# Optimization experiments

Hardware: AMD Instinct MI355X
Metric: run time of the kernel (lower is better)

The kernel has to match this reference:

```python
import jax, jax.numpy as jnp
import numpy as np

BN_EPS = 1e-5
LEAKY_SLOPE = 0.01

def setup_inputs() -> dict:
    key = jax.random.key(0)
    ks = jax.random.split(key, 8)
    B, N, C, D = 8, 2048, 128, 32  # batch, points, inchannels, outchannels
    s = 0.05
    return {
        "x": jax.random.normal(ks[0], (B, N, C), dtype=jnp.float32),
        "Wq": jax.random.normal(ks[1], (D, C), dtype=jnp.float32) * s,
        "Wk": jax.random.normal(ks[2], (D, C), dtype=jnp.float32) * s,
        "Wv": jax.random.normal(ks[3], (C, C), dtype=jnp.float32) * s,
        "Wp": jax.random.normal(ks[4], (C, C), dtype=jnp.float32) * s,
        "bn_gamma": jnp.ones((C,), dtype=jnp.float32),
        "bn_beta": jnp.zeros((C,), dtype=jnp.float32),
        "bn_mean": jax.random.normal(ks[5], (C,), dtype=jnp.float32) * 0.01,
        "bn_var": jnp.abs(jax.random.normal(ks[6], (C,), dtype=jnp.float32)) * 0.1 + 0.9,
    }

def reference(x, Wq, Wk, Wv, Wp, bn_gamma, bn_beta, bn_mean, bn_var):
    # x: [B, N, C]; 1x1 Conv1d == per-point linear map
    q = jnp.einsum('bnc,dc->bnd', x, Wq)          # [B, N, D]
    k = jnp.einsum('bnc,dc->bnd', x, Wk)          # [B, N, D]
    v = jnp.einsum('bnc,oc->bno', x, Wv)          # [B, N, C]
    energy = jnp.einsum('bnd,bmd->bnm', q, k)     # [B, Nq, Nk]
    # offset-attention: softmax over the QUERY axis (dim=1), then L1-renorm over keys
    attn = jax.nn.softmax(energy, axis=1)
    attn = attn / (1e-9 + attn.sum(axis=-1, keepdims=True))
    x_r = jnp.einsum('bnm,bmc->bnc', attn, v)     # [B, N, C]
    # project(x - x_r): 1x1 conv + BatchNorm (eval, running stats) + LeakyReLU; dropout p=0
    d = x - x_r
    y = jnp.einsum('bnc,oc->bno', d, Wp)
    y = (y - bn_mean) * (bn_gamma / jnp.sqrt(bn_var + BN_EPS)) + bn_beta
    y = jnp.where(y >= 0, y, LEAKY_SLOPE * y)
    return y + x
```

## Files before the change

kernel.cpp:

```cpp
#include <hip/hip_runtime.h>
#include <stdint.h>

#define BB 8
#define NN 2048
#define CC 128
#define DD 32
#define LOG2E 1.44269504088896340736f

typedef __attribute__((ext_vector_type(8))) short short8;
typedef __attribute__((ext_vector_type(4))) short short4v;
typedef __attribute__((ext_vector_type(4))) float f32x4;

#define MFMA(a,b,c) __builtin_amdgcn_mfma_f32_16x16x32_bf16(a,b,c,0,0,0)

__device__ __forceinline__ short f2b(float f){
  uint32_t u = __float_as_uint(f);
  uint32_t r = (u + 0x7fffu + ((u >> 16) & 1u)) >> 16;
  return (short)r;
}

__global__ void k_pack(const float* __restrict__ Wq, const float* __restrict__ Wk,
                       const float* __restrict__ Wv, const float* __restrict__ Wp,
                       const float* __restrict__ g, const float* __restrict__ bt,
                       const float* __restrict__ mu, const float* __restrict__ vr,
                       short* __restrict__ wqkv, short* __restrict__ wp,
                       float* __restrict__ scale, float* __restrict__ shift){
  int i = blockIdx.x*256 + threadIdx.x;
  if (i < 192*128){
    int r = i >> 7, c = i & 127;
    float w = (r < 32) ? Wq[r*128+c] : (r < 64) ? Wk[(r-32)*128+c] : Wv[(r-64)*128+c];
    wqkv[i] = f2b(w);
  }
  if (i < 128*128) wp[i] = f2b(Wp[i]);
  if (i < 128){
    float s = g[i] * rsqrtf(vr[i] + 1e-5f);
    scale[i] = s;
    shift[i] = bt[i] - mu[i]*s;
  }
}

__global__ __launch_bounds__(256,4) void k_qkv(const float* __restrict__ x, const short* __restrict__ wqkv,
    short* __restrict__ qb, short* __restrict__ kb, short* __restrict__ vt){
  const int tid = threadIdx.x;
  const int wv = tid >> 6, l = tid & 63, lrow = l & 15, lg = l >> 4;
  const int r0 = blockIdx.x*32 + (wv & 1)*16;
  const int base = (wv >> 1)*6;
  const float* xr = x + (long)(r0 + lrow)*CC;
  short8 a[4];
  #pragma unroll
  for (int ks=0; ks<4; ks++){
    f32x4 u0 = *(const f32x4*)(xr + ks*32 + lg*8);
    f32x4 u1 = *(const f32x4*)(xr + ks*32 + lg*8 + 4);
    short8 t;
    #pragma unroll
    for (int j=0;j<4;j++){ t[j] = f2b(u0[j]); t[4+j] = f2b(u1[j]); }
    a[ks] = t;
  }
  f32x4 acc[6];
  #pragma unroll
  for (int i=0;i<6;i++) acc[i] = f32x4{0.f,0.f,0.f,0.f};
  #pragma unroll
  for (int of=0; of<6; of++){
    #pragma unroll
    for (int ks=0; ks<4; ks++){
      short8 bfr = *(const short8*)(wqkv + ((base+of)*16 + lrow)*CC + ks*32 + lg*8);
      acc[of] = MFMA(a[ks], bfr, acc[of]);
    }
  }
  const int b = r0 / NN, nin = r0 % NN;
  #pragma unroll
  for (int of=0; of<6; of++){
    const int oo = base + of;
    const int o = oo*16 + lrow;
    if (oo < 2){
      #pragma unroll
      for (int rr=0; rr<4; rr++) qb[(long)(r0 + lg*4 + rr)*DD + o] = f2b(acc[of][rr]*LOG2E);
    } else if (oo < 4){
      #pragma unroll
      for (int rr=0; rr<4; rr++) kb[(long)(r0 + lg*4 + rr)*DD + (o-32)] = f2b(acc[of][rr]);
    } else {
      short4v s;
      #pragma unroll
      for (int rr=0; rr<4; rr++) s[rr] = f2b(acc[of][rr]);
      *(short4v*)(vt + (long)(b*CC + (o-64))*NN + nin + lg*4) = s;
    }
  }
}

__global__ __launch_bounds__(256,4) void k_colsum(const short* __restrict__ qb, const short* __restrict__ kb,
                                                  float* __restrict__ csum){
  const int tid = threadIdx.x;
  const int wv = tid >> 6, l = tid & 63, lrow = l & 15, lg = l >> 4;
  const int b = blockIdx.x >> 7;
  const int q = (blockIdx.x >> 5) & 3;
  const int m0 = (blockIdx.x & 31)*64 + wv*16;
  short8 afr = *(const short8*)(kb + (long)(b*NN + m0 + lrow)*DD + lg*8);
  const short* qbase = qb + (long)b*NN*DD;
  float sum[4] = {0.f,0.f,0.f,0.f};
  f32x4 z = {0.f,0.f,0.f,0.f};
  const int nbeg = q*512, nend = nbeg + 512;
  #pragma unroll 4
  for (int n0=nbeg; n0<nend; n0+=16){
    short8 bfr = *(const short8*)(qbase + (long)(n0 + lrow)*DD + lg*8);
    f32x4 e = MFMA(afr, bfr, z);
    #pragma unroll
    for (int r=0;r<4;r++) sum[r] += exp2f(e[r]);
  }
  #pragma unroll
  for (int mask=1; mask<16; mask<<=1){
    #pragma unroll
    for (int r=0;r<4;r++) sum[r] += __shfl_xor(sum[r], mask);
  }
  if (lrow == 0){
    #pragma unroll
    for (int r=0;r<4;r++) csum[q*(BB*NN) + b*NN + m0 + lg*4 + r] = sum[r];
  }
}

__global__ __launch_bounds__(256,4) void k_attn(const short* __restrict__ qb,
    const short* __restrict__ kb, const short* __restrict__ vt, const float* __restrict__ csum,
    float* __restrict__ accP, float* __restrict__ Lp){
  __shared__ __align__(16) short lds[17408];
  const int tid = threadIdx.x;
  const int wv = tid >> 6, l = tid & 63, lrow = l & 15, lg = l >> 4;
  const int b = blockIdx.x >> 7;
  const int quarter = (blockIdx.x >> 5) & 3;
  const int rt = blockIdx.x & 31;
  const int n0 = rt*64 + wv*16;
  short8 qfr = *(const short8*)(qb + (long)(b*NN + n0 + lrow)*DD + lg*8);
  const short* kbb = kb + (long)b*NN*DD;
  const short* vtb = vt + (long)b*CC*NN;
  float* sinvl = (float*)(lds + 16384);

  const int mbase = quarter*512;
  {
    const float* c0 = csum + b*NN + mbase;
    #pragma unroll
    for (int i=tid; i<512; i+=256){
      float s = c0[i] + c0[i + BB*NN] + c0[i + 2*BB*NN] + c0[i + 3*BB*NN];
      sinvl[i] = __builtin_amdgcn_rcpf(s);
    }
  }

  f32x4 acc[8];
  #pragma unroll
  for (int i=0;i<8;i++) acc[i] = f32x4{0.f,0.f,0.f,0.f};
  float L[4] = {0.f,0.f,0.f,0.f};

  short8 sv[4]; short8 sk[2];
  const int cr = tid >> 1, hf = tid & 1;

  auto loadT = [&](int m0){
    const short* s = vtb + (long)cr*NN + m0 + hf*32;
    sv[0] = *(const short8*)(s);
    sv[1] = *(const short8*)(s+8);
    sv[2] = *(const short8*)(s+16);
    sv[3] = *(const short8*)(s+24);
    if (tid < 128){
      const short* s2 = kbb + (long)(m0 + cr)*DD + hf*16;
      sk[0] = *(const short8*)(s2);
      sk[1] = *(const short8*)(s2+8);
    }
  };
  auto storeT = [&](){
    short* vt_t = lds;
    *(short8*)(vt_t + cr*72 + hf*32 + 0)  = sv[0];
    *(short8*)(vt_t + cr*72 + hf*32 + 8)  = sv[1];
    *(short8*)(vt_t + cr*72 + hf*32 + 16) = sv[2];
    *(short8*)(vt_t + cr*72 + hf*32 + 24) = sv[3];
    if (tid < 128){
      short* kb_t = vt_t + 9216;
      *(short8*)(kb_t + cr*40 + hf*16 + 0) = sk[0];
      *(short8*)(kb_t + cr*40 + hf*16 + 8) = sk[1];
    }
  };

  loadT(mbase);
  storeT();
  __syncthreads();

  short* pl = lds + 11776 + wv*1152;
  f32x4 z = {0.f,0.f,0.f,0.f};
  for (int it=0; it<8; it++){
    const int m0 = mbase + it*64;
    if (it < 7) loadT(m0 + 64);
    short* vt_t = lds;
    short* kb_t = lds + 9216;
    float p[16];
    #pragma unroll
    for (int mt=0; mt<4; mt++){
      short8 bfr = *(short8*)(kb_t + (mt*16 + lrow)*40 + lg*8);
      f32x4 e = MFMA(qfr, bfr, z);
      float si = sinvl[it*64 + mt*16 + lrow];
      #pragma unroll
      for (int r=0;r<4;r++) p[mt*4+r] = exp2f(e[r]) * si;
    }
    #pragma unroll
    for (int r=0;r<4;r++) L[r] += (p[r] + p[4+r]) + (p[8+r] + p[12+r]);
    #pragma unroll
    for (int mt=0; mt<4; mt++){
      #pragma unroll
      for (int r=0;r<4;r++)
        pl[(lg*4+r)*72 + mt*16 + lrow] = f2b(p[mt*4+r]);
    }
    __builtin_amdgcn_s_setprio(1);
    #pragma unroll
    for (int ks=0; ks<2; ks++){
      short8 pa = *(short8*)(pl + lrow*72 + ks*32 + lg*8);
      #pragma unroll
      for (int cf=0; cf<8; cf++){
        short8 vb_ = *(short8*)(vt_t + (cf*16 + lrow)*72 + ks*32 + lg*8);
        acc[cf] = MFMA(pa, vb_, acc[cf]);
      }
    }
    __builtin_amdgcn_s_setprio(0);
    __syncthreads();
    if (it < 7){
      storeT();
      __syncthreads();
    }
  }

  #pragma unroll
  for (int mask=1; mask<16; mask<<=1){
    #pragma unroll
    for (int r=0;r<4;r++) L[r] += __shfl_xor(L[r], mask);
  }

  const long tile = (long)((b*32 + rt)*4 + quarter);
  float* aP = accP + tile*64*128;
  #pragma unroll
  for (int cf=0; cf<8; cf++){
    #pragma unroll
    for (int r=0;r<4;r++)
      aP[(wv*16 + lg*4 + r)*128 + cf*16 + lrow] = acc[cf][r];
  }
  if (lrow == 0){
    #pragma unroll
    for (int r=0;r<4;r++) Lp[tile*64 + wv*16 + lg*4 + r] = L[r];
  }
}

__global__ __launch_bounds__(256,4) void k_fin(const float* __restrict__ x, const float* __restrict__ accP,
    const float* __restrict__ Lp, const short* __restrict__ wp, const float* __restrict__ scale,
    const float* __restrict__ shift, float* __restrict__ out){
  __shared__ __align__(16) short lds[4352];
  const int tid = threadIdx.x;
  const int wv = tid >> 6, l = tid & 63, lrow = l & 15, lg = l >> 4;
  const int b = blockIdx.x >> 6;
  const int rt = blockIdx.x & 63;
  const int rh = wv >> 1, ch = wv & 1;
  const int nb = rt*32 + rh*16;

  float linv[4];
  #pragma unroll
  for (int r=0;r<4;r++){
    const int n = nb + lg*4 + r;
    const long tb = ((long)(b*32 + (n>>6))*4)*64 + (n & 63);
    float Ls = Lp[tb] + Lp[tb+64] + Lp[tb+128] + Lp[tb+192];
    linv[r] = __builtin_amdgcn_rcpf(1e-9f + Ls);
  }

  short* dl = lds + rh*2176;
  float xv[16];
  #pragma unroll
  for (int cf=0; cf<4; cf++){
    #pragma unroll
    for (int r=0;r<4;r++){
      const int n = nb + lg*4 + r;
      const int col = ch*64 + cf*16 + lrow;
      float xx = x[((long)(b*NN + n))*CC + col];
      xv[cf*4+r] = xx;
      const long ab = (((long)(b*32 + (n>>6))*4)*64 + (n & 63))*128 + col;
      float a = accP[ab] + accP[ab + 64*128] + accP[ab + 2*64*128] + accP[ab + 3*64*128];
      dl[(lg*4+r)*136 + col] = f2b(xx - a*linv[r]);
    }
  }
  __syncthreads();

  f32x4 yac[4];
  #pragma unroll
  for (int i=0;i<4;i++) yac[i] = f32x4{0.f,0.f,0.f,0.f};
  #pragma unroll
  for (int ks=0; ks<4; ks++){
    short8 da = *(short8*)(dl + lrow*136 + ks*32 + lg*8);
    #pragma unroll
    for (int of=0; of<4; of++){
      short8 wfr = *(const short8*)(wp + ((ch*4+of)*16 + lrow)*CC + ks*32 + lg*8);
      yac[of] = MFMA(da, wfr, yac[of]);
    }
  }
  float* ob = out + ((long)(b*NN + nb))*CC;
  #pragma unroll
  for (int of=0; of<4; of++){
    const int o = (ch*4+of)*16 + lrow;
    const float sc = scale[o], sh = shift[o];
    #pragma unroll
    for (int r=0;r<4;r++){
      float y = yac[of][r]*sc + sh;
      y = (y >= 0.f) ? y : 0.01f*y;
      ob[(lg*4+r)*CC + o] = y + xv[of*4+r];
    }
  }
}

__global__ __launch_bounds__(256) void k_attn_mono(const float* __restrict__ x, const short* __restrict__ qb,
    const short* __restrict__ kb, const short* __restrict__ vt, const float* __restrict__ csum,
    const short* __restrict__ wp, const float* __restrict__ scale, const float* __restrict__ shift,
    float* __restrict__ out){
  __shared__ __align__(16) short lds[28160];
  const int tid = threadIdx.x;
  const int wv = tid >> 6, l = tid & 63, lrow = l & 15, lg = l >> 4;
  const int b = blockIdx.x >> 5;
  const int n0 = (blockIdx.x & 31)*64 + wv*16;
  short8 qfr = *(const short8*)(qb + (long)(b*NN + n0 + lrow)*DD + lg*8);
  const short* kbb = kb + (long)b*NN*DD;
  const short* vtb = vt + (long)b*CC*NN;
  const float* c0 = csum + b*NN;

  f32x4 acc[8];
  #pragma unroll
  for (int i=0;i<8;i++) acc[i] = f32x4{0.f,0.f,0.f,0.f};
  float L[4] = {0.f,0.f,0.f,0.f};
  short8 sv[4]; short8 sk[2];
  const int cr = tid >> 1, hf = tid & 1;
  auto loadT = [&](int m0){
    const short* s = vtb + (long)cr*NN + m0 + hf*32;
    sv[0] = *(const short8*)(s); sv[1] = *(const short8*)(s+8);
    sv[2] = *(const short8*)(s+16); sv[3] = *(const short8*)(s+24);
    if (tid < 128){
      const short* s2 = kbb + (long)(m0 + cr)*DD + hf*16;
      sk[0] = *(const short8*)(s2); sk[1] = *(const short8*)(s2+8);
    }
  };
  auto storeT = [&](int buf){
    short* vt_t = lds + buf*11776;
    *(short8*)(vt_t + cr*72 + hf*32 + 0)  = sv[0];
    *(short8*)(vt_t + cr*72 + hf*32 + 8)  = sv[1];
    *(short8*)(vt_t + cr*72 + hf*32 + 16) = sv[2];
    *(short8*)(vt_t + cr*72 + hf*32 + 24) = sv[3];
    if (tid < 128){
      short* kb_t = vt_t + 9216;
      *(short8*)(kb_t + cr*40 + hf*16 + 0) = sk[0];
      *(short8*)(kb_t + cr*40 + hf*16 + 8) = sk[1];
    }
  };
  loadT(0); storeT(0); __syncthreads();
  short* pl = lds + 23552 + wv*1152;
  f32x4 z = {0.f,0.f,0.f,0.f};
  for (int it=0; it<32; it++){
    const int m0 = it*64;
    const int cur = it & 1;
    if (it < 31) loadT(m0 + 64);
    short* vt_t = lds + cur*11776;
    short* kb_t = vt_t + 9216;
    float p[16];
    #pragma unroll
    for (int mt=0; mt<4; mt++){
      short8 bfr = *(short8*)(kb_t + (mt*16 + lrow)*40 + lg*8);
      f32x4 e = MFMA(qfr, bfr, z);
      const int m = m0 + mt*16 + lrow;
      float si = __builtin_amdgcn_rcpf(c0[m] + c0[m+BB*NN] + c0[m+2*BB*NN] + c0[m+3*BB*NN]);
      #pragma unroll
      for (int r=0;r<4;r++) p[mt*4+r] = exp2f(e[r]) * si;
    }
    #pragma unroll
    for (int r=0;r<4;r++) L[r] += (p[r] + p[4+r]) + (p[8+r] + p[12+r]);
    #pragma unroll
    for (int mt=0; mt<4; mt++){
      #pragma unroll
      for (int r=0;r<4;r++)
        pl[(lg*4+r)*72 + mt*16 + lrow] = f2b(p[mt*4+r]);
    }
    #pragma unroll
    for (int ks=0; ks<2; ks++){
      short8 pa = *(short8*)(pl + lrow*72 + ks*32 + lg*8);
      #pragma unroll
      for (int cf=0; cf<8; cf++){
        short8 vb_ = *(short8*)(vt_t + (cf*16 + lrow)*72 + ks*32 + lg*8);
        acc[cf] = MFMA(pa, vb_, acc[cf]);
      }
    }
    if (it < 31) storeT((it+1) & 1);
    __syncthreads();
  }
  #pragma unroll
  for (int mask=1; mask<16; mask<<=1){
    #pragma unroll
    for (int r=0;r<4;r++) L[r] += __shfl_xor(L[r], mask);
  }
  float linv[4];
  #pragma unroll
  for (int r=0;r<4;r++) linv[r] = __builtin_amdgcn_rcpf(1e-9f + L[r]);
  const float* xbb = x + (long)(b*NN + n0)*CC;
  float xv[32];
  short* dl = lds + wv*2176;
  #pragma unroll
  for (int cf=0; cf<8; cf++){
    #pragma unroll
    for (int r=0;r<4;r++){
      float xx = xbb[(lg*4+r)*CC + cf*16 + lrow];
      xv[cf*4+r] = xx;
      dl[(lg*4+r)*136 + cf*16 + lrow] = f2b(xx - acc[cf][r]*linv[r]);
    }
  }
  f32x4 yac[8];
  #pragma unroll
  for (int i=0;i<8;i++) yac[i] = f32x4{0.f,0.f,0.f,0.f};
  #pragma unroll
  for (int ks=0; ks<4; ks++){
    short8 da = *(short8*)(dl + lrow*136 + ks*32 + lg*8);
    #pragma unroll
    for (int of=0; of<8; of++){
      short8 wfr = *(const short8*)(wp + (of*16 + lrow)*CC + ks*32 + lg*8);
      yac[of] = MFMA(da, wfr, yac[of]);
    }
  }
  float* ob = out + (long)(b*NN + n0)*CC;
  #pragma unroll
  for (int of=0; of<8; of++){
    const int o = of*16 + lrow;
    const float sc = scale[o], sh = shift[o];
    #pragma unroll
    for (int r=0;r<4;r++){
      float y = yac[of][r]*sc + sh;
      y = (y >= 0.f) ? y : 0.01f*y;
      ob[(lg*4+r)*CC + o] = y + xv[of*4+r];
    }
  }
}

extern "C" void kernel_launch(void* const* d_in, const int* in_sizes, int n_in,
                              void* d_out, int out_size, void* d_ws, size_t ws_size,
                              hipStream_t stream) {
  const float* x  = (const float*)d_in[0];
  const float* Wq = (const float*)d_in[1];
  const float* Wk = (const float*)d_in[2];
  const float* Wv = (const float*)d_in[3];
  const float* Wp = (const float*)d_in[4];
  const float* g  = (const float*)d_in[5];
  const float* bt = (const float*)d_in[6];
  const float* mu = (const float*)d_in[7];
  const float* vr = (const float*)d_in[8];
  float* out = (float*)d_out;

  char* ws = (char*)d_ws;
  short* wqkv  = (short*)(ws + 0);
  short* wp    = (short*)(ws + 49152);
  float* scale = (float*)(ws + 81920);
  float* shift = (float*)(ws + 82432);
  short* qb    = (short*)(ws + 98304);
  short* kb    = (short*)(ws + 1146880);
  short* vt    = (short*)(ws + 2195456);
  float* csum  = (float*)(ws + 6389760);
  float* Lp    = (float*)(ws + 6651904);
  float* accP  = (float*)(ws + 6914048);
  const size_t need_split = 6914048 + 33554432;

  k_pack<<<96, 256, 0, stream>>>(Wq, Wk, Wv, Wp, g, bt, mu, vr, wqkv, wp, scale, shift);
  k_qkv<<<512, 256, 0, stream>>>(x, wqkv, qb, kb, vt);
  k_colsum<<<1024, 256, 0, stream>>>(qb, kb, csum);
  if (ws_size >= need_split){
    k_attn<<<1024, 256, 0, stream>>>(qb, kb, vt, csum, accP, Lp);
    k_fin<<<512, 256, 0, stream>>>(x, accP, Lp, wp, scale, shift, out);
  } else {
    k_attn_mono<<<256, 256, 0, stream>>>(x, qb, kb, vt, csum, wp, scale, shift, out);
  }
}
```

Baseline: 133.9 us.

## Store attention partials as bf16, regrid qkv/fin kernels, reorder block mapping

The split-K attention partial accumulators are now written and read as bf16 instead of fp32, halving that intermediate buffer's traffic. k_fin is rewritten to use one 16-row tile per block, with vectorized coalesced loads of the partials and x. k_qkv is regridded to twice as many smaller blocks. Block index mapping in k_colsum and k_attn is reordered so neighbouring blocks span batches and quarters. The bf16 partials add rounding error before the four-way sum, and x is re-read in the epilogue.

```diff
diff --git a/kernel.cpp b/kernel.cpp
--- a/kernel.cpp
+++ b/kernel.cpp
@@ -17,6 +17,10 @@
   uint32_t u = __float_as_uint(f);
   uint32_t r = (u + 0x7fffu + ((u >> 16) & 1u)) >> 16;
   return (short)r;
+}
+__device__ __forceinline__ float b2f(short s){
+  uint32_t u = ((uint32_t)(uint16_t)s) << 16;
+  return __uint_as_float(u);
 }
 
 __global__ void k_pack(const float* __restrict__ Wq, const float* __restrict__ Wk,
@@ -43,8 +47,8 @@
     short* __restrict__ qb, short* __restrict__ kb, short* __restrict__ vt){
   const int tid = threadIdx.x;
   const int wv = tid >> 6, l = tid & 63, lrow = l & 15, lg = l >> 4;
-  const int r0 = blockIdx.x*32 + (wv & 1)*16;
-  const int base = (wv >> 1)*6;
+  const int r0 = blockIdx.x*16;
+  const int base = wv*3;
   const float* xr = x + (long)(r0 + lrow)*CC;
   short8 a[4];
   #pragma unroll
@@ -56,11 +60,11 @@
     for (int j=0;j<4;j++){ t[j] = f2b(u0[j]); t[4+j] = f2b(u1[j]); }
     a[ks] = t;
   }
-  f32x4 acc[6];
-  #pragma unroll
-  for (int i=0;i<6;i++) acc[i] = f32x4{0.f,0.f,0.f,0.f};
-  #pragma unroll
-  for (int of=0; of<6; of++){
+  f32x4 acc[3];
+  #pragma unroll
+  for (int i=0;i<3;i++) acc[i] = f32x4{0.f,0.f,0.f,0.f};
+  #pragma unroll
+  for (int of=0; of<3; of++){
     #pragma unroll
     for (int ks=0; ks<4; ks++){
       short8 bfr = *(const short8*)(wqkv + ((base+of)*16 + lrow)*CC + ks*32 + lg*8);
@@ -69,7 +73,7 @@
   }
   const int b = r0 / NN, nin = r0 % NN;
   #pragma unroll
-  for (int of=0; of<6; of++){
+  for (int of=0; of<3; of++){
     const int oo = base + of;
     const int o = oo*16 + lrow;
     if (oo < 2){
@@ -91,9 +95,9 @@
                                                   float* __restrict__ csum){
   const int tid = threadIdx.x;
   const int wv = tid >> 6, l = tid & 63, lrow = l & 15, lg = l >> 4;
-  const int b = blockIdx.x >> 7;
-  const int q = (blockIdx.x >> 5) & 3;
-  const int m0 = (blockIdx.x & 31)*64 + wv*16;
+  const int bq = blockIdx.x & 31;
+  const int b = bq >> 2, q = bq & 3;
+  const int m0 = (blockIdx.x >> 5)*64 + wv*16;
   short8 afr = *(const short8*)(kb + (long)(b*NN + m0 + lrow)*DD + lg*8);
   const short* qbase = qb + (long)b*NN*DD;
   float sum[4] = {0.f,0.f,0.f,0.f};
@@ -119,13 +123,14 @@
 
 __global__ __launch_bounds__(256,4) void k_attn(const short* __restrict__ qb,
     const short* __restrict__ kb, const short* __restrict__ vt, const float* __restrict__ csum,
-    float* __restrict__ accP, float* __restrict__ Lp){
+    short* __restrict__ accPb, float* __restrict__ Lp){
   __shared__ __align__(16) short lds[17408];
   const int tid = threadIdx.x;
   const int wv = tid >> 6, l = tid & 63, lrow = l & 15, lg = l >> 4;
-  const int b = blockIdx.x >> 7;
-  const int quarter = (blockIdx.x >> 5) & 3;
-  const int rt = blockIdx.x & 31;
+  const int bq = blockIdx.x & 31;
+  const int b = bq >> 2;
+  const int quarter = bq & 3;
+  const int rt = blockIdx.x >> 5;
   const int n0 = rt*64 + wv*16;
   short8 qfr = *(const short8*)(qb + (long)(b*NN + n0 + lrow)*DD + lg*8);
   const short* kbb = kb + (long)b*NN*DD;
@@ -228,12 +233,12 @@
   }
 
   const long tile = (long)((b*32 + rt)*4 + quarter);
-  float* aP = accP + tile*64*128;
+  short* aP = accPb + tile*64*128;
   #pragma unroll
   for (int cf=0; cf<8; cf++){
     #pragma unroll
     for (int r=0;r<4;r++)
-      aP[(wv*16 + lg*4 + r)*128 + cf*16 + lrow] = acc[cf][r];
+      aP[(wv*16 + lg*4 + r)*128 + cf*16 + lrow] = f2b(acc[cf][r]);
   }
   if (lrow == 0){
     #pragma unroll
@@ -241,65 +246,76 @@
   }
 }
 
-__global__ __launch_bounds__(256,4) void k_fin(const float* __restrict__ x, const float* __restrict__ accP,
+__global__ __launch_bounds__(256,4) void k_fin(const float* __restrict__ x, const short* __restrict__ accPb,
     const float* __restrict__ Lp, const short* __restrict__ wp, const float* __restrict__ scale,
     const float* __restrict__ shift, float* __restrict__ out){
-  __shared__ __align__(16) short lds[4352];
+  __shared__ __align__(16) short dl[16*136];
+  __shared__ float linv_s[16];
   const int tid = threadIdx.x;
   const int wv = tid >> 6, l = tid & 63, lrow = l & 15, lg = l >> 4;
-  const int b = blockIdx.x >> 6;
-  const int rt = blockIdx.x & 63;
-  const int rh = wv >> 1, ch = wv & 1;
-  const int nb = rt*32 + rh*16;
-
-  float linv[4];
-  #pragma unroll
-  for (int r=0;r<4;r++){
-    const int n = nb + lg*4 + r;
-    const long tb = ((long)(b*32 + (n>>6))*4)*64 + (n & 63);
-    float Ls = Lp[tb] + Lp[tb+64] + Lp[tb+128] + Lp[tb+192];
-    linv[r] = __builtin_amdgcn_rcpf(1e-9f + Ls);
-  }
-
-  short* dl = lds + rh*2176;
-  float xv[16];
-  #pragma unroll
-  for (int cf=0; cf<4; cf++){
-    #pragma unroll
-    for (int r=0;r<4;r++){
-      const int n = nb + lg*4 + r;
-      const int col = ch*64 + cf*16 + lrow;
-      float xx = x[((long)(b*NN + n))*CC + col];
-      xv[cf*4+r] = xx;
-      const long ab = (((long)(b*32 + (n>>6))*4)*64 + (n & 63))*128 + col;
-      float a = accP[ab] + accP[ab + 64*128] + accP[ab + 2*64*128] + accP[ab + 3*64*128];
-      dl[(lg*4+r)*136 + col] = f2b(xx - a*linv[r]);
-    }
-  }
+  const int b = blockIdx.x >> 7;
+  const int rt = blockIdx.x & 127;
+  const int nb = rt*16;
+  const long tileIdx = (long)(b*32 + (rt>>2))*4;
+  const int rowoff = (rt&3)*16;
+
+  if (tid < 16){
+    float Ls = Lp[(tileIdx+0)*64 + rowoff + tid] + Lp[(tileIdx+1)*64 + rowoff + tid]
+             + Lp[(tileIdx+2)*64 + rowoff + tid] + Lp[(tileIdx+3)*64 + rowoff + tid];
+    linv_s[tid] = __builtin_amdgcn_rcpf(1e-9f + Ls);
+  }
+
+  const int row_l = tid >> 4;
+  const int c0 = (tid & 15)*8;
+  float a[8];
+  #pragma unroll
+  for (int j=0;j<8;j++) a[j] = 0.f;
+  #pragma unroll
+  for (int p=0;p<4;p++){
+    short8 v = *(const short8*)(accPb + (tileIdx+p)*64*128 + (rowoff+row_l)*128 + c0);
+    #pragma unroll
+    for (int j=0;j<8;j++) a[j] += b2f(v[j]);
+  }
+  const float* xr = x + ((long)(b*NN + nb + row_l))*CC + c0;
+  f32x4 x0 = *(const f32x4*)(xr);
+  f32x4 x1 = *(const f32x4*)(xr + 4);
   __syncthreads();
-
-  f32x4 yac[4];
-  #pragma unroll
-  for (int i=0;i<4;i++) yac[i] = f32x4{0.f,0.f,0.f,0.f};
+  {
+    const float li = linv_s[row_l];
+    short4v d0, d1;
+    #pragma unroll
+    for (int j=0;j<4;j++){
+      d0[j] = f2b(x0[j] - a[j]*li);
+      d1[j] = f2b(x1[j] - a[4+j]*li);
+    }
+    *(short4v*)(dl + row_l*136 + c0) = d0;
+    *(short4v*)(dl + row_l*136 + c0 + 4) = d1;
+  }
+  __syncthreads();
+
+  f32x4 yac[2];
+  yac[0] = f32x4{0.f,0.f,0.f,0.f};
+  yac[1] = f32x4{0.f,0.f,0.f,0.f};
   #pragma unroll
   for (int ks=0; ks<4; ks++){
     short8 da = *(short8*)(dl + lrow*136 + ks*32 + lg*8);
     #pragma unroll
-    for (int of=0; of<4; of++){
-      short8 wfr = *(const short8*)(wp + ((ch*4+of)*16 + lrow)*CC + ks*32 + lg*8);
+    for (int of=0; of<2; of++){
+      short8 wfr = *(const short8*)(wp + ((wv*2+of)*16 + lrow)*CC + ks*32 + lg*8);
       yac[of] = MFMA(da, wfr, yac[of]);
     }
   }
   float* ob = out + ((long)(b*NN + nb))*CC;
-  #pragma unroll
-  for (int of=0; of<4; of++){
-    const int o = (ch*4+of)*16 + lrow;
+  const float* xb = x + ((long)(b*NN + nb))*CC;
+  #pragma unroll
+  for (int of=0; of<2; of++){
+    const int o = (wv*2+of)*16 + lrow;
     const float sc = scale[o], sh = shift[o];
     #pragma unroll
     for (int r=0;r<4;r++){
       float y = yac[of][r]*sc + sh;
       y = (y >= 0.f) ? y : 0.01f*y;
-      ob[(lg*4+r)*CC + o] = y + xv[of*4+r];
+      ob[(lg*4+r)*CC + o] = y + xb[(lg*4+r)*CC + o];
     }
   }
 }
@@ -454,15 +470,15 @@
   short* vt    = (short*)(ws + 2195456);
   float* csum  = (float*)(ws + 6389760);
   float* Lp    = (float*)(ws + 6651904);
-  float* accP  = (float*)(ws + 6914048);
-  const size_t need_split = 6914048 + 33554432;
+  short* accPb = (short*)(ws + 6914048);
+  const size_t need_split = 6914048 + 16777216;
 
   k_pack<<<96, 256, 0, stream>>>(Wq, Wk, Wv, Wp, g, bt, mu, vr, wqkv, wp, scale, shift);
-  k_qkv<<<512, 256, 0, stream>>>(x, wqkv, qb, kb, vt);
+  k_qkv<<<1024, 256, 0, stream>>>(x, wqkv, qb, kb, vt);
   k_colsum<<<1024, 256, 0, stream>>>(qb, kb, csum);
   if (ws_size >= need_split){
-    k_attn<<<1024, 256, 0, stream>>>(qb, kb, vt, csum, accP, Lp);
-    k_fin<<<512, 256, 0, stream>>>(x, accP, Lp, wp, scale, shift, out);
+    k_attn<<<1024, 256, 0, stream>>>(qb, kb, vt, csum, accPb, Lp);
+    k_fin<<<1024, 256, 0, stream>>>(x, accPb, Lp, wp, scale, shift, out);
   } else {
     k_attn_mono<<<256, 256, 0, stream>>>(x, qb, kb, vt, csum, wp, scale, shift, out);
   }
```

Result: faster. 131.2 us (-2.0%).
